# Performance work log

Hardware: AMD Instinct MI355X
Metric: run time of the kernel (lower is better)

Reference implementation:

```python
import jax, jax.numpy as jnp
import numpy as np

N = 8192          # num atoms
K = 32            # neighbors per atom (init kwarg k)
CUTOFF = 10.0     # init kwarg cutoff
NUM_MOLS = 128


def setup_inputs() -> dict:
    key = jax.random.key(0)
    k1, k2 = jax.random.split(key)
    pos = jax.random.normal(k1, (N, 3), dtype=jnp.float32)
    batch = jnp.sort(jax.random.randint(k2, (N,), 0, NUM_MOLS)).astype(jnp.int32)
    return {"pos": pos, "batch": batch}


def _pairwise_dist(pos):
    # ||x_i - x_j|| via the gram-matrix expansion; avoids an [N,N,3] intermediate.
    sq_norm = jnp.sum(pos * pos, axis=-1)                     # [N]
    sq = sq_norm[:, None] + sq_norm[None, :] - 2.0 * (pos @ pos.T)  # [N,N]
    sq = jnp.maximum(sq, 0.0)
    # safe sqrt: exact 0 on the diagonal without nan-producing sqrt'(0) in grads
    safe = jnp.where(sq > 0, sq, 1.0)
    return jnp.where(sq > 0, jnp.sqrt(safe), 0.0)


def reference(pos, batch):
    n = pos.shape[0]
    pdist = _pairwise_dist(pos)                               # [N,N]
    rows = jnp.arange(n)
    diag = rows[:, None] == rows[None, :]
    cross = batch[:, None] != batch[None, :]
    outer = pdist > CUTOFF
    mask = diag | cross | outer
    pdist = jnp.where(mask, CUTOFF, pdist)
    neg_w, indices = jax.lax.top_k(-pdist, K)                 # [N,K] each
    rows_e = jnp.broadcast_to(rows[:, None], indices.shape)
    edge_index = jnp.stack([indices.reshape(-1), rows_e.reshape(-1)])  # [2, N*K]
    edge_weight = -neg_w.reshape(-1)                          # [N*K]
    return edge_index, edge_weight
```

## Files before the change

kernel.cpp:

```cpp
#include <hip/hip_runtime.h>


#define CUTOFF_F 10.0f
#define SDMAX 256
#define ROWS_PER_BLOCK 4

__device__ __forceinline__ float dist_v(float4 pr, float4 pc, bool diag) {
    if (diag) return CUTOFF_F;
    float dot = __fadd_rn(__fadd_rn(__fmul_rn(pr.x, pc.x), __fmul_rn(pr.y, pc.y)),
                          __fmul_rn(pr.z, pc.z));
    float sq = __fsub_rn(__fadd_rn(pr.w, pc.w), __fadd_rn(dot, dot));
    sq = fmaxf(sq, 0.0f);
    float d = (sq > 0.0f) ? __fsqrt_rn(sq) : 0.0f;
    return (d > CUTOFF_F) ? CUTOFF_F : d;
}

__device__ __forceinline__ float4 load_pos4(const float* __restrict__ pos, int g) {
    float x = pos[g * 3 + 0];
    float y = pos[g * 3 + 1];
    float z = pos[g * 3 + 2];
    float sq = __fadd_rn(__fadd_rn(__fmul_rn(x, x), __fmul_rn(y, y)), __fmul_rn(z, z));
    return make_float4(x, y, z, sq);
}

template <typename MaskF>
__device__ __forceinline__ void do_fill(int m, int K, int lane, int start, int end,
                                        int n, int r, int NK,
                                        float* __restrict__ out, MaskF masked_at) {
    const int mm = n - m;
    for (int fbase = 0; fbase < K - m; fbase += 64) {
        const int t = fbase + lane;
        const bool active = t < (K - m);
        int idx = 0;
        bool found = false;
        if (active) {
            if (t < start)              { idx = t;                        found = true; }
            else if (t - start >= mm)   { idx = end + (t - start - mm);   found = true; }
        }
        if (__any(active && !found)) {
            int cnt = 0;
            for (int cc = 0; cc < n; ++cc) {
                if (masked_at(cc)) {
                    if (active && !found && cnt == t - start) { idx = start + cc; found = true; }
                    ++cnt;
                }
            }
        }
        if (active) {
            int o = r * K + m + t;
            out[o]          = (float)idx;
            out[2 * NK + o] = CUTOFF_F;
        }
    }
}

template <int NCH>
__device__ __forceinline__ void row_core(const float* __restrict__ srow, int n,
                                         int lane, int start, int end, int r,
                                         float* __restrict__ out, int NK, int K) {
    float vr[NCH];
    int   rk[NCH];
#pragma unroll
    for (int j = 0; j < NCH; ++j) {
        int c = lane + 64 * j;
        vr[j] = (c < n) ? srow[c] : CUTOFF_F;
        rk[j] = 0;
    }
#pragma unroll 4
    for (int cc = 0; cc < n; ++cc) {
        float vv = srow[cc];
#pragma unroll
        for (int j = 0; j < NCH; ++j) {
            int c = lane + 64 * j;
            rk[j] += (vv < vr[j]) || (vv == vr[j] && cc < c);
        }
    }
    int m = 0;
#pragma unroll
    for (int j = 0; j < NCH; ++j) {
        int c = lane + 64 * j;
        m += __popcll(__ballot(c < n && vr[j] < CUTOFF_F));
    }
#pragma unroll
    for (int j = 0; j < NCH; ++j) {
        int c = lane + 64 * j;
        if (c < n && vr[j] < CUTOFF_F && rk[j] < K) {
            int o = r * K + rk[j];
            out[o]          = (float)(start + c);
            out[2 * NK + o] = vr[j];
        }
    }
    for (int k2 = lane; k2 < K; k2 += 64)
        out[NK + r * K + k2] = (float)r;
    if (m < K)
        do_fill(m, K, lane, start, end, n, r, NK, out,
                [&](int cc) { return srow[cc] == CUTOFF_F; });
}

__global__ __launch_bounds__(256)
void knn_rows_kernel(const float* __restrict__ pos,
                     const int* __restrict__ batch,
                     float* __restrict__ out,
                     int N, int K) {
    __shared__ float sd[ROWS_PER_BLOCK][SDMAX];
    const int w    = threadIdx.x >> 6;
    const int lane = threadIdx.x & 63;
    const int r = min(blockIdx.x * ROWS_PER_BLOCK + w, N - 1);
    const int NK = N * K;

    const int b = batch[r];
    int lo = 0, hi = r;
    while (lo < hi) { int mid = (lo + hi) >> 1; if (batch[mid] < b) lo = mid + 1; else hi = mid; }
    const int start = lo;
    lo = r + 1; hi = N;
    while (lo < hi) { int mid = (lo + hi) >> 1; if (batch[mid] < b + 1) lo = mid + 1; else hi = mid; }
    const int end = lo;
    const int n = end - start;

    const float4 pr = load_pos4(pos, r);
    const bool lds_ok = (n <= SDMAX);

    if (lds_ok) {
        float* srow = sd[w];
        for (int c = lane; c < n; c += 64)
            srow[c] = dist_v(pr, load_pos4(pos, start + c), (start + c) == r);
    }
    __syncthreads();

    if (lds_ok) {
        const float* srow = sd[w];
        if (n <= 64)        row_core<1>(srow, n, lane, start, end, r, out, NK, K);
        else if (n <= 128)  row_core<2>(srow, n, lane, start, end, r, out, NK, K);
        else                row_core<4>(srow, n, lane, start, end, r, out, NK, K);
    } else {
        int m = 0;
        for (int cbase = 0; cbase < n; cbase += 64) {
            const int c = cbase + lane;
            float v = (c < n) ? dist_v(pr, load_pos4(pos, start + c), (start + c) == r)
                              : CUTOFF_F;
            int rk = 0;
            for (int cc = 0; cc < n; ++cc) {
                float vv = dist_v(pr, load_pos4(pos, start + cc), (start + cc) == r);
                rk += (vv < v) || (vv == v && cc < c);
            }
            if (c < n && v < CUTOFF_F && rk < K) {
                int o = r * K + rk;
                out[o]          = (float)(start + c);
                out[2 * NK + o] = v;
            }
            m += __popcll(__ballot(c < n && v < CUTOFF_F));
        }
        for (int k2 = lane; k2 < K; k2 += 64)
            out[NK + r * K + k2] = (float)r;
        if (m < K)
            do_fill(m, K, lane, start, end, n, r, NK, out, [&](int cc) {
                return dist_v(pr, load_pos4(pos, start + cc), (start + cc) == r) == CUTOFF_F;
            });
    }
}

extern "C" void kernel_launch(void* const* d_in, const int* in_sizes, int n_in,
                              void* d_out, int out_size, void* d_ws, size_t ws_size,
                              hipStream_t stream) {
    const float* pos   = (const float*)d_in[0];
    const int*   batch = (const int*)d_in[1];
    float*       out   = (float*)d_out;

    const int N = in_sizes[1];
    const int K = out_size / (3 * N);

    const int grid = (N + ROWS_PER_BLOCK - 1) / ROWS_PER_BLOCK;
    knn_rows_kernel<<<grid, 256, 0, stream>>>(pos, batch, out, N, K);
}
```

Measured before the change: 72.72 us.

## Keep row distances in registers with readlane broadcast and precompute molecule bounds

Each wavefront now keeps its row's distances in VGPRs and broadcasts them with readlane for the rank count, instead of staging them through LDS with a block barrier. A new prepass kernel writes per-molecule start offsets into the workspace and fills the row-index part of the output, replacing the two binary searches per row. The main kernel gains a launch-bounds occupancy hint and no longer needs shared memory. In exchange there is a second kernel launch, and the code hardcodes NUM_MOLS=128 when sizing the offset table.

```diff
diff --git a/kernel.cpp b/kernel.cpp
--- a/kernel.cpp
+++ b/kernel.cpp
@@ -2,8 +2,12 @@
 
 
 #define CUTOFF_F 10.0f
-#define SDMAX 256
+#define NUM_MOLS 128
 #define ROWS_PER_BLOCK 4
+
+__device__ __forceinline__ float readlane_f(float v, int lane) {
+    return __int_as_float(__builtin_amdgcn_readlane(__float_as_int(v), lane));
+}
 
 __device__ __forceinline__ float dist_v(float4 pr, float4 pc, bool diag) {
     if (diag) return CUTOFF_F;
@@ -23,139 +27,172 @@
     return make_float4(x, y, z, sq);
 }
 
-template <typename MaskF>
-__device__ __forceinline__ void do_fill(int m, int K, int lane, int start, int end,
-                                        int n, int r, int NK,
-                                        float* __restrict__ out, MaskF masked_at) {
-    const int mm = n - m;
-    for (int fbase = 0; fbase < K - m; fbase += 64) {
-        const int t = fbase + lane;
-        const bool active = t < (K - m);
-        int idx = 0;
-        bool found = false;
-        if (active) {
-            if (t < start)              { idx = t;                        found = true; }
-            else if (t - start >= mm)   { idx = end + (t - start - mm);   found = true; }
-        }
-        if (__any(active && !found)) {
-            int cnt = 0;
-            for (int cc = 0; cc < n; ++cc) {
-                if (masked_at(cc)) {
-                    if (active && !found && cnt == t - start) { idx = start + cc; found = true; }
-                    ++cnt;
-                }
-            }
-        }
-        if (active) {
-            int o = r * K + m + t;
-            out[o]          = (float)idx;
-            out[2 * NK + o] = CUTOFF_F;
-        }
+__global__ __launch_bounds__(256)
+void knn_prepass(const int* __restrict__ batch, int* __restrict__ ms,
+                 float* __restrict__ out, int N, int K) {
+    const int t = blockIdx.x * blockDim.x + threadIdx.x;
+    const int NK = N * K;
+    if (t < NK) out[NK + t] = (float)(t / K);
+    if (t < N) {
+        const int bi = batch[t];
+        const int bp = (t == 0) ? -1 : batch[t - 1];
+        for (int b = bp + 1; b <= bi; ++b) ms[b] = t;
+        if (t == N - 1)
+            for (int b = bi + 1; b <= NUM_MOLS; ++b) ms[b] = N;
     }
 }
 
 template <int NCH>
-__device__ __forceinline__ void row_core(const float* __restrict__ srow, int n,
-                                         int lane, int start, int end, int r,
-                                         float* __restrict__ out, int NK, int K) {
-    float vr[NCH];
+__device__ __forceinline__ void row_core_reg(const float* __restrict__ pos,
+                                             float4 pr, int n, int lane,
+                                             int start, int end, int r,
+                                             float* __restrict__ out,
+                                             int NK, int K) {
+    float v[NCH];
     int   rk[NCH];
 #pragma unroll
     for (int j = 0; j < NCH; ++j) {
-        int c = lane + 64 * j;
-        vr[j] = (c < n) ? srow[c] : CUTOFF_F;
+        const int c = 64 * j + lane;
+        v[j]  = (c < n) ? dist_v(pr, load_pos4(pos, start + c), (start + c) == r)
+                        : CUTOFF_F;
         rk[j] = 0;
     }
+#pragma unroll
+    for (int jj = 0; jj < NCH; ++jj) {
+        const int base = 64 * jj;
+        const int lim  = (NCH == 1) ? n : min(n - base, 64);
 #pragma unroll 4
-    for (int cc = 0; cc < n; ++cc) {
-        float vv = srow[cc];
-#pragma unroll
-        for (int j = 0; j < NCH; ++j) {
-            int c = lane + 64 * j;
-            rk[j] += (vv < vr[j]) || (vv == vr[j] && cc < c);
+        for (int cc = 0; cc < lim; ++cc) {
+            const float vv = readlane_f(v[jj], cc);
+            const int   g  = base + cc;
+#pragma unroll
+            for (int j = 0; j < NCH; ++j) {
+                const int c = 64 * j + lane;
+                rk[j] += (vv < v[j]) || (vv == v[j] && g < c);
+            }
         }
     }
     int m = 0;
 #pragma unroll
     for (int j = 0; j < NCH; ++j) {
-        int c = lane + 64 * j;
-        m += __popcll(__ballot(c < n && vr[j] < CUTOFF_F));
+        const int c = 64 * j + lane;
+        m += __popcll(__ballot(c < n && v[j] < CUTOFF_F));
     }
 #pragma unroll
     for (int j = 0; j < NCH; ++j) {
-        int c = lane + 64 * j;
-        if (c < n && vr[j] < CUTOFF_F && rk[j] < K) {
-            int o = r * K + rk[j];
+        const int c = 64 * j + lane;
+        if (c < n && v[j] < CUTOFF_F && rk[j] < K) {
+            const int o = r * K + rk[j];
             out[o]          = (float)(start + c);
-            out[2 * NK + o] = vr[j];
-        }
-    }
-    for (int k2 = lane; k2 < K; k2 += 64)
-        out[NK + r * K + k2] = (float)r;
-    if (m < K)
-        do_fill(m, K, lane, start, end, n, r, NK, out,
-                [&](int cc) { return srow[cc] == CUTOFF_F; });
-}
-
-__global__ __launch_bounds__(256)
+            out[2 * NK + o] = v[j];
+        }
+    }
+    if (m < K) {
+        const int mm = n - m;
+        for (int fb = 0; fb < K - m; fb += 64) {
+            const int t = fb + lane;
+            const bool active = t < (K - m);
+            int idx = 0;
+            bool found = false;
+            if (active) {
+                if (t < start)            { idx = t;                      found = true; }
+                else if (t - start >= mm) { idx = end + (t - start - mm); found = true; }
+            }
+            if (__any(active && !found)) {
+                int cnt = 0;
+#pragma unroll
+                for (int jj = 0; jj < NCH; ++jj) {
+                    const int base = 64 * jj;
+                    const int lim  = min(n - base, 64);
+                    for (int cc = 0; cc < lim; ++cc) {
+                        if (readlane_f(v[jj], cc) == CUTOFF_F) {
+                            if (active && !found && cnt == t - start) {
+                                idx = start + base + cc; found = true;
+                            }
+                            ++cnt;
+                        }
+                    }
+                }
+            }
+            if (active) {
+                const int o = r * K + m + t;
+                out[o]          = (float)idx;
+                out[2 * NK + o] = CUTOFF_F;
+            }
+        }
+    }
+}
+
+__global__ __launch_bounds__(256, 8)
 void knn_rows_kernel(const float* __restrict__ pos,
                      const int* __restrict__ batch,
+                     const int* __restrict__ ms,
                      float* __restrict__ out,
                      int N, int K) {
-    __shared__ float sd[ROWS_PER_BLOCK][SDMAX];
     const int w    = threadIdx.x >> 6;
     const int lane = threadIdx.x & 63;
-    const int r = min(blockIdx.x * ROWS_PER_BLOCK + w, N - 1);
+    const int r    = blockIdx.x * ROWS_PER_BLOCK + w;
+    if (r >= N) return;
     const int NK = N * K;
 
-    const int b = batch[r];
-    int lo = 0, hi = r;
-    while (lo < hi) { int mid = (lo + hi) >> 1; if (batch[mid] < b) lo = mid + 1; else hi = mid; }
-    const int start = lo;
-    lo = r + 1; hi = N;
-    while (lo < hi) { int mid = (lo + hi) >> 1; if (batch[mid] < b + 1) lo = mid + 1; else hi = mid; }
-    const int end = lo;
-    const int n = end - start;
+    const int b     = batch[r];
+    const int start = ms[b];
+    const int end   = ms[b + 1];
+    const int n     = end - start;
 
     const float4 pr = load_pos4(pos, r);
-    const bool lds_ok = (n <= SDMAX);
-
-    if (lds_ok) {
-        float* srow = sd[w];
-        for (int c = lane; c < n; c += 64)
-            srow[c] = dist_v(pr, load_pos4(pos, start + c), (start + c) == r);
-    }
-    __syncthreads();
-
-    if (lds_ok) {
-        const float* srow = sd[w];
-        if (n <= 64)        row_core<1>(srow, n, lane, start, end, r, out, NK, K);
-        else if (n <= 128)  row_core<2>(srow, n, lane, start, end, r, out, NK, K);
-        else                row_core<4>(srow, n, lane, start, end, r, out, NK, K);
-    } else {
+
+    if      (n <= 64)  row_core_reg<1>(pos, pr, n, lane, start, end, r, out, NK, K);
+    else if (n <= 128) row_core_reg<2>(pos, pr, n, lane, start, end, r, out, NK, K);
+    else if (n <= 192) row_core_reg<3>(pos, pr, n, lane, start, end, r, out, NK, K);
+    else if (n <= 256) row_core_reg<4>(pos, pr, n, lane, start, end, r, out, NK, K);
+    else {
         int m = 0;
-        for (int cbase = 0; cbase < n; cbase += 64) {
-            const int c = cbase + lane;
-            float v = (c < n) ? dist_v(pr, load_pos4(pos, start + c), (start + c) == r)
-                              : CUTOFF_F;
+        for (int cb = 0; cb < n; cb += 64) {
+            const int c = cb + lane;
+            const float v = (c < n)
+                ? dist_v(pr, load_pos4(pos, start + c), (start + c) == r) : CUTOFF_F;
             int rk = 0;
             for (int cc = 0; cc < n; ++cc) {
-                float vv = dist_v(pr, load_pos4(pos, start + cc), (start + cc) == r);
+                const float vv = dist_v(pr, load_pos4(pos, start + cc), (start + cc) == r);
                 rk += (vv < v) || (vv == v && cc < c);
             }
             if (c < n && v < CUTOFF_F && rk < K) {
-                int o = r * K + rk;
+                const int o = r * K + rk;
                 out[o]          = (float)(start + c);
                 out[2 * NK + o] = v;
             }
             m += __popcll(__ballot(c < n && v < CUTOFF_F));
         }
-        for (int k2 = lane; k2 < K; k2 += 64)
-            out[NK + r * K + k2] = (float)r;
-        if (m < K)
-            do_fill(m, K, lane, start, end, n, r, NK, out, [&](int cc) {
-                return dist_v(pr, load_pos4(pos, start + cc), (start + cc) == r) == CUTOFF_F;
-            });
+        if (m < K) {
+            const int mm = n - m;
+            for (int fb = 0; fb < K - m; fb += 64) {
+                const int t = fb + lane;
+                const bool active = t < (K - m);
+                int idx = 0; bool found = false;
+                if (active) {
+                    if (t < start)            { idx = t;                      found = true; }
+                    else if (t - start >= mm) { idx = end + (t - start - mm); found = true; }
+                }
+                if (__any(active && !found)) {
+                    int cnt = 0;
+                    for (int cc = 0; cc < n; ++cc) {
+                        if (dist_v(pr, load_pos4(pos, start + cc), (start + cc) == r)
+                            == CUTOFF_F) {
+                            if (active && !found && cnt == t - start) {
+                                idx = start + cc; found = true;
+                            }
+                            ++cnt;
+                        }
+                    }
+                }
+                if (active) {
+                    const int o = r * K + m + t;
+                    out[o]          = (float)idx;
+                    out[2 * NK + o] = CUTOFF_F;
+                }
+            }
+        }
     }
 }
 
@@ -165,10 +202,14 @@
     const float* pos   = (const float*)d_in[0];
     const int*   batch = (const int*)d_in[1];
     float*       out   = (float*)d_out;
+    int*         ms    = (int*)d_ws;
 
     const int N = in_sizes[1];
     const int K = out_size / (3 * N);
 
-    const int grid = (N + ROWS_PER_BLOCK - 1) / ROWS_PER_BLOCK;
-    knn_rows_kernel<<<grid, 256, 0, stream>>>(pos, batch, out, N, K);
-}
+    const int gridA = (N * K + 255) / 256;
+    knn_prepass<<<gridA, 256, 0, stream>>>(batch, ms, out, N, K);
+
+    const int gridB = (N + ROWS_PER_BLOCK - 1) / ROWS_PER_BLOCK;
+    knn_rows_kernel<<<gridB, 256, 0, stream>>>(pos, batch, ms, out, N, K);
+}
```

Result: faster. 67.67 us (-6.9%).
